# Kernel tuning notes

Hardware: AMD Instinct MI355X
Metric: run time of the kernel (lower is better)

Reference implementation:

```python
import jax, jax.numpy as jnp
import numpy as np
from jax import lax

DN = ('NCHW', 'OIHW', 'NCHW')

def _score(x, dw_w, dw_b, pw_w, pw_b):
    C = x.shape[1]
    # depthwise 3x3 conv (groups=C), padding=1
    h = lax.conv_general_dilated(x, dw_w, (1, 1), 'SAME', dimension_numbers=DN,
                                 feature_group_count=C)
    h = h + dw_b[None, :, None, None]
    # 1x1 conv C->1
    s = lax.conv_general_dilated(h, pw_w, (1, 1), 'SAME', dimension_numbers=DN)
    s = s + pw_b[None, :, None, None]
    return jax.nn.sigmoid(s)  # [B,1,H,W]


def setup_inputs() -> dict:
    key = jax.random.key(0)
    ks = jax.random.split(key, 8)
    B, C, H, W = 8, 64, 256, 256
    inp = {
        'x0': jax.random.normal(ks[0], (B, C, H, W), jnp.float32),
        'x1': jax.random.normal(ks[1], (B, C, H, W), jnp.float32),
        'dw_w0': jax.random.normal(ks[2], (C, 1, 3, 3), jnp.float32) * 0.1,
        'dw_b0': jnp.zeros((C,), jnp.float32),
        'pw_w0': jax.random.normal(ks[3], (1, C, 1, 1), jnp.float32) * 0.1,
        'pw_b0': jnp.zeros((1,), jnp.float32),
        'dw_w1': jax.random.normal(ks[4], (C, 1, 3, 3), jnp.float32) * 0.1,
        'dw_b1': jnp.zeros((C,), jnp.float32),
        'pw_w1': jax.random.normal(ks[5], (1, C, 1, 1), jnp.float32) * 0.1,
        'pw_b1': jnp.zeros((1,), jnp.float32),
    }
    return inp


def reference(x0, x1, dw_w0, dw_b0, pw_w0, pw_b0, dw_w1, dw_b1, pw_w1, pw_b1):
    s0 = _score(x0, dw_w0, dw_b0, pw_w0, pw_b0)  # [B,1,H,W]
    s1 = _score(x1, dw_w1, dw_b1, pw_w1, pw_b1)
    w0 = s0 * x0 + x0  # [B,C,H,W]
    w1 = s1 * x1 + x1
    stacked = jnp.stack([w0, w1])            # [2,B,C,H,W]
    idx = jnp.argmax(stacked, axis=0)        # [B,C,H,W] int
    x_f = jnp.where(idx == 0, x0, x1)
    percentages = jnp.stack([jnp.mean((idx == i).astype(jnp.float32)) for i in range(2)])
    return x_f, percentages
```

## Files before the change

kernel.cpp:

```cpp
#include <hip/hip_runtime.h>
#include <math.h>
#include <stdint.h>

#define B 8
#define C 64
#define H 256
#define W 256
#define PSZ (H * W)

#define OFF_WC    256
#define OFF_BIAS  9728

__global__ void prep_kernel(const float* __restrict__ dw_w0, const float* __restrict__ dw_b0,
                            const float* __restrict__ pw_w0, const float* __restrict__ pw_b0,
                            const float* __restrict__ dw_w1, const float* __restrict__ dw_b1,
                            const float* __restrict__ pw_w1, const float* __restrict__ pw_b1,
                            double* __restrict__ wc, double* __restrict__ bias)
{
    int t = threadIdx.x;
    int which = t >> 6, c = t & 63;
    const float* dw = which ? dw_w1 : dw_w0;
    const float* pw = which ? pw_w1 : pw_w0;
    double p = (double)pw[c];
    #pragma unroll
    for (int k = 0; k < 9; ++k)
        wc[(which * 64 + c) * 9 + k] = p * (double)dw[c * 9 + k];
    if (c == 0) {
        const float* dwb = which ? dw_b1 : dw_b0;
        const float* pwb = which ? pw_b1 : pw_b0;
        double acc = (double)pwb[0];
        for (int cc = 0; cc < 64; ++cc) acc += (double)pw[cc] * (double)dwb[cc];
        bias[which] = acc;
    }
}

template<int JLO, int JHI>
__device__ __forceinline__ void ch_compute(
    float4 r0, float4 r1, float4 r2, float4 r3,
    const double* __restrict__ wl9,
    int lane, double acc[2][4])
{
    double wl[9];
    #pragma unroll
    for (int t = 0; t < 9; ++t) wl[t] = wl9[t];

    const float4 rr[4] = {r0, r1, r2, r3};
    #pragma unroll
    for (int j = 0; j < 4; ++j) {
        if (j < JLO || j > JHI) continue;
        float lf = __shfl_up(rr[j].w, 1);
        float rf = __shfl_down(rr[j].x, 1);
        if (lane == 0)  lf = 0.0f;
        if (lane == 63) rf = 0.0f;
        double dd[6] = {(double)lf, (double)rr[j].x, (double)rr[j].y,
                        (double)rr[j].z, (double)rr[j].w, (double)rf};
        #pragma unroll
        for (int i = 0; i < 3; ++i) {
            const int o = j - i;
            if (o >= 0 && o < 2) {
                double wa = wl[3 * i], wb = wl[3 * i + 1], wcv = wl[3 * i + 2];
                #pragma unroll
                for (int k = 0; k < 4; ++k)
                    acc[o][k] += wa * dd[k] + wb * dd[k + 1] + wcv * dd[k + 2];
            }
        }
    }
}

template<int JLO, int JHI>
__device__ __forceinline__ void accum_q(
    const float* __restrict__ xb,
    const double* __restrict__ w9,
    const int gy[4], int lane, double acc[2][4])
{
    #pragma unroll 1
    for (int cc = 0; cc < 16; cc += 2) {
        const float* xcA = xb + (size_t)cc * PSZ;
        const float* xcB = xcA + PSZ;
        float4 a0 = *(const float4*)(xcA + gy[0]);
        float4 a1 = *(const float4*)(xcA + gy[1]);
        float4 a2 = *(const float4*)(xcA + gy[2]);
        float4 a3 = *(const float4*)(xcA + gy[3]);
        float4 b0 = *(const float4*)(xcB + gy[0]);
        float4 b1 = *(const float4*)(xcB + gy[1]);
        float4 b2 = *(const float4*)(xcB + gy[2]);
        float4 b3 = *(const float4*)(xcB + gy[3]);
        __builtin_amdgcn_sched_barrier(0);
        ch_compute<JLO, JHI>(a0, a1, a2, a3, w9 + cc * 9, lane, acc);
        ch_compute<JLO, JHI>(b0, b1, b2, b3, w9 + (cc + 1) * 9, lane, acc);
    }
}

__global__ __launch_bounds__(512) void fused_kernel(
    const float* __restrict__ x0, const float* __restrict__ x1,
    const double* __restrict__ wc, const double* __restrict__ bias,
    float* __restrict__ out, unsigned int* __restrict__ count1)
{
    __shared__ double sred[2][4][2][4][64];
    __shared__ unsigned int scnt;

    const int n    = blockIdx.x;
    const int task = (n & 7) * 128 + (n >> 3);
    const int b    = task >> 7;
    const int band = task & 127;
    const int y0   = band * 2;

    const int tid   = threadIdx.x;
    const int w     = tid >> 6;
    const int lane  = tid & 63;
    const int which = w >> 2;
    const int chunk = w & 3;

    if (tid == 0) scnt = 0;

    const float* xin = which ? x1 : x0;
    const float* xb  = xin + (size_t)b * C * PSZ + (size_t)(chunk * 16) * PSZ + lane * 4;
    const double* w9 = wc + which * (C * 9) + (chunk * 16) * 9;

    int gy[4];
    #pragma unroll
    for (int j = 0; j < 4; ++j) {
        int r = y0 - 1 + j;
        r = r < 0 ? 0 : (r > H - 1 ? H - 1 : r);
        gy[j] = r * W;
    }

    double acc[2][4] = {};

    if (band == 0)        accum_q<1, 3>(xb, w9, gy, lane, acc);
    else if (band == 127) accum_q<0, 2>(xb, w9, gy, lane, acc);
    else                  accum_q<0, 3>(xb, w9, gy, lane, acc);

    #pragma unroll
    for (int o = 0; o < 2; ++o)
        #pragma unroll
        for (int k = 0; k < 4; ++k)
            sred[which][chunk][o][k][lane] = acc[o][k];
    __syncthreads();

    double fv0, fv1;
    {
        int idx = tid;
        int wh = idx >> 9, row = (idx >> 8) & 1, px = idx & 255;
        int k = px & 3, l = px >> 2;
        double s = sred[wh][0][row][k][l] + sred[wh][1][row][k][l]
                 + sred[wh][2][row][k][l] + sred[wh][3][row][k][l] + bias[wh];
        fv0 = 1.0 + 1.0 / (1.0 + exp(-s));
    }
    {
        int idx = 512 + tid;
        int wh = idx >> 9, row = (idx >> 8) & 1, px = idx & 255;
        int k = px & 3, l = px >> 2;
        double s = sred[wh][0][row][k][l] + sred[wh][1][row][k][l]
                 + sred[wh][2][row][k][l] + sred[wh][3][row][k][l] + bias[wh];
        fv1 = 1.0 + 1.0 / (1.0 + exp(-s));
    }
    __syncthreads();

    double* sf = &sred[0][0][0][0][0];
    sf[tid] = fv0;
    sf[512 + tid] = fv1;
    __syncthreads();

    const int tx = tid & 63;
    const int tc = tid >> 6;

    double g0[2][4], g1[2][4];
    #pragma unroll
    for (int row = 0; row < 2; ++row)
        #pragma unroll
        for (int j = 0; j < 4; ++j) {
            g0[row][j] = sf[row * 256 + tx * 4 + j];
            g1[row][j] = sf[512 + row * 256 + tx * 4 + j];
        }

    unsigned int cnt = 0;
    const size_t base = (size_t)b * C * PSZ + (size_t)y0 * W + (size_t)tx * 4;
    #pragma unroll 1
    for (int ci = tc; ci < C; ci += 8) {
        #pragma unroll
        for (int row = 0; row < 2; ++row) {
            size_t off = base + (size_t)ci * PSZ + (size_t)row * W;
            float4 a  = *(const float4*)(x0 + off);
            float4 bb = *(const float4*)(x1 + off);
            float4 r;
            { double v0=(double)a.x*g0[row][0], v1=(double)bb.x*g1[row][0]; bool s1=(v1>v0); cnt+=s1; r.x=s1?bb.x:a.x; }
            { double v0=(double)a.y*g0[row][1], v1=(double)bb.y*g1[row][1]; bool s1=(v1>v0); cnt+=s1; r.y=s1?bb.y:a.y; }
            { double v0=(double)a.z*g0[row][2], v1=(double)bb.z*g1[row][2]; bool s1=(v1>v0); cnt+=s1; r.z=s1?bb.z:a.z; }
            { double v0=(double)a.w*g0[row][3], v1=(double)bb.w*g1[row][3]; bool s1=(v1>v0); cnt+=s1; r.w=s1?bb.w:a.w; }
            *(float4*)(out + off) = r;
        }
    }

    atomicAdd(&scnt, cnt);
    __syncthreads();
    if (tid == 0) atomicAdd(count1, scnt);
}

__global__ void finalize_kernel(const unsigned int* __restrict__ count1,
                                float* __restrict__ out_p)
{
    const double N = (double)B * C * H * W;
    double c1 = (double)(*count1);
    out_p[0] = (float)((N - c1) / N);
    out_p[1] = (float)(c1 / N);
}

extern "C" void kernel_launch(void* const* d_in, const int* in_sizes, int n_in,
                              void* d_out, int out_size, void* d_ws, size_t ws_size,
                              hipStream_t stream) {
    const float* x0    = (const float*)d_in[0];
    const float* x1    = (const float*)d_in[1];
    const float* dw_w0 = (const float*)d_in[2];
    const float* dw_b0 = (const float*)d_in[3];
    const float* pw_w0 = (const float*)d_in[4];
    const float* pw_b0 = (const float*)d_in[5];
    const float* dw_w1 = (const float*)d_in[6];
    const float* dw_b1 = (const float*)d_in[7];
    const float* pw_w1 = (const float*)d_in[8];
    const float* pw_b1 = (const float*)d_in[9];
    float* out = (float*)d_out;

    unsigned int* cnt  = (unsigned int*)d_ws;
    double*       wc   = (double*)((char*)d_ws + OFF_WC);
    double*       bias = (double*)((char*)d_ws + OFF_BIAS);

    (void)hipMemsetAsync(d_ws, 0, 256, stream);

    prep_kernel<<<1, 128, 0, stream>>>(dw_w0, dw_b0, pw_w0, pw_b0,
                                       dw_w1, dw_b1, pw_w1, pw_b1, wc, bias);

    fused_kernel<<<B * (H / 2), 512, 0, stream>>>(x0, x1, wc, bias, out, cnt);

    finalize_kernel<<<1, 1, 0, stream>>>(cnt, out + (size_t)B * C * H * W);
}
```

Before: 129.9 us.

## Process one output row per block with 256 threads instead of two rows

Each block now handles a single output row with 256 threads (2 waves per input, 32 channels each) instead of two rows with 512 threads, and the grid doubles. This shrinks registers and shared memory per block and raises the number of blocks available for scheduling. In exchange, halo reuse drops: each output row now reads 3 input rows instead of 4 for 2 rows, so the score pass does more global loads per output.

```diff
diff --git a/kernel.cpp b/kernel.cpp
--- a/kernel.cpp
+++ b/kernel.cpp
@@ -36,17 +36,13 @@
 
 template<int JLO, int JHI>
 __device__ __forceinline__ void ch_compute(
-    float4 r0, float4 r1, float4 r2, float4 r3,
+    float4 r0, float4 r1, float4 r2,
     const double* __restrict__ wl9,
-    int lane, double acc[2][4])
-{
-    double wl[9];
-    #pragma unroll
-    for (int t = 0; t < 9; ++t) wl[t] = wl9[t];
-
-    const float4 rr[4] = {r0, r1, r2, r3};
-    #pragma unroll
-    for (int j = 0; j < 4; ++j) {
+    int lane, double acc[4])
+{
+    const float4 rr[3] = {r0, r1, r2};
+    #pragma unroll
+    for (int j = 0; j < 3; ++j) {
         if (j < JLO || j > JHI) continue;
         float lf = __shfl_up(rr[j].w, 1);
         float rf = __shfl_down(rr[j].x, 1);
@@ -54,16 +50,10 @@
         if (lane == 63) rf = 0.0f;
         double dd[6] = {(double)lf, (double)rr[j].x, (double)rr[j].y,
                         (double)rr[j].z, (double)rr[j].w, (double)rf};
+        double wa = wl9[3 * j], wb = wl9[3 * j + 1], wcv = wl9[3 * j + 2];
         #pragma unroll
-        for (int i = 0; i < 3; ++i) {
-            const int o = j - i;
-            if (o >= 0 && o < 2) {
-                double wa = wl[3 * i], wb = wl[3 * i + 1], wcv = wl[3 * i + 2];
-                #pragma unroll
-                for (int k = 0; k < 4; ++k)
-                    acc[o][k] += wa * dd[k] + wb * dd[k + 1] + wcv * dd[k + 2];
-            }
-        }
+        for (int k = 0; k < 4; ++k)
+            acc[k] += wa * dd[k] + wb * dd[k + 1] + wcv * dd[k + 2];
     }
 }
 
@@ -71,125 +61,113 @@
 __device__ __forceinline__ void accum_q(
     const float* __restrict__ xb,
     const double* __restrict__ w9,
-    const int gy[4], int lane, double acc[2][4])
+    const int gy[3], int lane, double acc[4])
 {
     #pragma unroll 1
-    for (int cc = 0; cc < 16; cc += 2) {
+    for (int cc = 0; cc < 32; cc += 2) {
         const float* xcA = xb + (size_t)cc * PSZ;
         const float* xcB = xcA + PSZ;
         float4 a0 = *(const float4*)(xcA + gy[0]);
         float4 a1 = *(const float4*)(xcA + gy[1]);
         float4 a2 = *(const float4*)(xcA + gy[2]);
-        float4 a3 = *(const float4*)(xcA + gy[3]);
         float4 b0 = *(const float4*)(xcB + gy[0]);
         float4 b1 = *(const float4*)(xcB + gy[1]);
         float4 b2 = *(const float4*)(xcB + gy[2]);
-        float4 b3 = *(const float4*)(xcB + gy[3]);
         __builtin_amdgcn_sched_barrier(0);
-        ch_compute<JLO, JHI>(a0, a1, a2, a3, w9 + cc * 9, lane, acc);
-        ch_compute<JLO, JHI>(b0, b1, b2, b3, w9 + (cc + 1) * 9, lane, acc);
-    }
-}
-
-__global__ __launch_bounds__(512) void fused_kernel(
+        ch_compute<JLO, JHI>(a0, a1, a2, w9 + cc * 9, lane, acc);
+        ch_compute<JLO, JHI>(b0, b1, b2, w9 + (cc + 1) * 9, lane, acc);
+    }
+}
+
+__global__ __launch_bounds__(256) void fused_kernel(
     const float* __restrict__ x0, const float* __restrict__ x1,
     const double* __restrict__ wc, const double* __restrict__ bias,
     float* __restrict__ out, unsigned int* __restrict__ count1)
 {
-    __shared__ double sred[2][4][2][4][64];
+    __shared__ double sred[2][2][4][64];
     __shared__ unsigned int scnt;
 
     const int n    = blockIdx.x;
-    const int task = (n & 7) * 128 + (n >> 3);
-    const int b    = task >> 7;
-    const int band = task & 127;
-    const int y0   = band * 2;
+    const int task = (n & 7) * 256 + (n >> 3);
+    const int b    = task >> 8;
+    const int y    = task & 255;
 
     const int tid   = threadIdx.x;
     const int w     = tid >> 6;
     const int lane  = tid & 63;
-    const int which = w >> 2;
-    const int chunk = w & 3;
+    const int which = w >> 1;
+    const int chunk = w & 1;
 
     if (tid == 0) scnt = 0;
 
     const float* xin = which ? x1 : x0;
-    const float* xb  = xin + (size_t)b * C * PSZ + (size_t)(chunk * 16) * PSZ + lane * 4;
-    const double* w9 = wc + which * (C * 9) + (chunk * 16) * 9;
-
-    int gy[4];
-    #pragma unroll
-    for (int j = 0; j < 4; ++j) {
-        int r = y0 - 1 + j;
+    const float* xb  = xin + (size_t)b * C * PSZ + (size_t)(chunk * 32) * PSZ + lane * 4;
+    const double* w9 = wc + which * (C * 9) + (chunk * 32) * 9;
+
+    int gy[3];
+    #pragma unroll
+    for (int j = 0; j < 3; ++j) {
+        int r = y - 1 + j;
         r = r < 0 ? 0 : (r > H - 1 ? H - 1 : r);
         gy[j] = r * W;
     }
 
-    double acc[2][4] = {};
-
-    if (band == 0)        accum_q<1, 3>(xb, w9, gy, lane, acc);
-    else if (band == 127) accum_q<0, 2>(xb, w9, gy, lane, acc);
-    else                  accum_q<0, 3>(xb, w9, gy, lane, acc);
-
-    #pragma unroll
-    for (int o = 0; o < 2; ++o)
-        #pragma unroll
-        for (int k = 0; k < 4; ++k)
-            sred[which][chunk][o][k][lane] = acc[o][k];
+    double acc[4] = {};
+
+    if (y == 0)            accum_q<1, 2>(xb, w9, gy, lane, acc);
+    else if (y == H - 1)   accum_q<0, 1>(xb, w9, gy, lane, acc);
+    else                   accum_q<0, 2>(xb, w9, gy, lane, acc);
+
+    #pragma unroll
+    for (int k = 0; k < 4; ++k)
+        sred[which][chunk][k][lane] = acc[k];
     __syncthreads();
 
     double fv0, fv1;
     {
         int idx = tid;
-        int wh = idx >> 9, row = (idx >> 8) & 1, px = idx & 255;
+        int wh = idx >> 8, px = idx & 255;
         int k = px & 3, l = px >> 2;
-        double s = sred[wh][0][row][k][l] + sred[wh][1][row][k][l]
-                 + sred[wh][2][row][k][l] + sred[wh][3][row][k][l] + bias[wh];
+        double s = sred[wh][0][k][l] + sred[wh][1][k][l] + bias[wh];
         fv0 = 1.0 + 1.0 / (1.0 + exp(-s));
     }
     {
-        int idx = 512 + tid;
-        int wh = idx >> 9, row = (idx >> 8) & 1, px = idx & 255;
+        int idx = 256 + tid;
+        int wh = idx >> 8, px = idx & 255;
         int k = px & 3, l = px >> 2;
-        double s = sred[wh][0][row][k][l] + sred[wh][1][row][k][l]
-                 + sred[wh][2][row][k][l] + sred[wh][3][row][k][l] + bias[wh];
+        double s = sred[wh][0][k][l] + sred[wh][1][k][l] + bias[wh];
         fv1 = 1.0 + 1.0 / (1.0 + exp(-s));
     }
     __syncthreads();
 
-    double* sf = &sred[0][0][0][0][0];
+    double* sf = &sred[0][0][0][0];
     sf[tid] = fv0;
-    sf[512 + tid] = fv1;
+    sf[256 + tid] = fv1;
     __syncthreads();
 
     const int tx = tid & 63;
     const int tc = tid >> 6;
 
-    double g0[2][4], g1[2][4];
-    #pragma unroll
-    for (int row = 0; row < 2; ++row)
-        #pragma unroll
-        for (int j = 0; j < 4; ++j) {
-            g0[row][j] = sf[row * 256 + tx * 4 + j];
-            g1[row][j] = sf[512 + row * 256 + tx * 4 + j];
-        }
+    double g0[4], g1[4];
+    #pragma unroll
+    for (int j = 0; j < 4; ++j) {
+        g0[j] = sf[tx * 4 + j];
+        g1[j] = sf[256 + tx * 4 + j];
+    }
 
     unsigned int cnt = 0;
-    const size_t base = (size_t)b * C * PSZ + (size_t)y0 * W + (size_t)tx * 4;
+    const size_t base = (size_t)b * C * PSZ + (size_t)y * W + (size_t)tx * 4;
     #pragma unroll 1
-    for (int ci = tc; ci < C; ci += 8) {
-        #pragma unroll
-        for (int row = 0; row < 2; ++row) {
-            size_t off = base + (size_t)ci * PSZ + (size_t)row * W;
-            float4 a  = *(const float4*)(x0 + off);
-            float4 bb = *(const float4*)(x1 + off);
-            float4 r;
-            { double v0=(double)a.x*g0[row][0], v1=(double)bb.x*g1[row][0]; bool s1=(v1>v0); cnt+=s1; r.x=s1?bb.x:a.x; }
-            { double v0=(double)a.y*g0[row][1], v1=(double)bb.y*g1[row][1]; bool s1=(v1>v0); cnt+=s1; r.y=s1?bb.y:a.y; }
-            { double v0=(double)a.z*g0[row][2], v1=(double)bb.z*g1[row][2]; bool s1=(v1>v0); cnt+=s1; r.z=s1?bb.z:a.z; }
-            { double v0=(double)a.w*g0[row][3], v1=(double)bb.w*g1[row][3]; bool s1=(v1>v0); cnt+=s1; r.w=s1?bb.w:a.w; }
-            *(float4*)(out + off) = r;
-        }
+    for (int ci = tc; ci < C; ci += 4) {
+        size_t off = base + (size_t)ci * PSZ;
+        float4 a  = *(const float4*)(x0 + off);
+        float4 bb = *(const float4*)(x1 + off);
+        float4 r;
+        { double v0=(double)a.x*g0[0], v1=(double)bb.x*g1[0]; bool s1=(v1>v0); cnt+=s1; r.x=s1?bb.x:a.x; }
+        { double v0=(double)a.y*g0[1], v1=(double)bb.y*g1[1]; bool s1=(v1>v0); cnt+=s1; r.y=s1?bb.y:a.y; }
+        { double v0=(double)a.z*g0[2], v1=(double)bb.z*g1[2]; bool s1=(v1>v0); cnt+=s1; r.z=s1?bb.z:a.z; }
+        { double v0=(double)a.w*g0[3], v1=(double)bb.w*g1[3]; bool s1=(v1>v0); cnt+=s1; r.w=s1?bb.w:a.w; }
+        *(float4*)(out + off) = r;
     }
 
     atomicAdd(&scnt, cnt);
@@ -230,7 +208,7 @@
     prep_kernel<<<1, 128, 0, stream>>>(dw_w0, dw_b0, pw_w0, pw_b0,
                                        dw_w1, dw_b1, pw_w1, pw_b1, wc, bias);
 
-    fused_kernel<<<B * (H / 2), 512, 0, stream>>>(x0, x1, wc, bias, out, cnt);
+    fused_kernel<<<B * H, 256, 0, stream>>>(x0, x1, wc, bias, out, cnt);
 
     finalize_kernel<<<1, 1, 0, stream>>>(cnt, out + (size_t)B * C * H * W);
 }
```

New measurement: 164.9 us. +27.0%, slower.
